# Performance work log

Hardware: AMD Instinct MI355X
Metric: run time of the kernel (lower is better)

The kernel has to match this reference:

```python
import jax, jax.numpy as jnp
import numpy as np
import math

# ---- static config (matches init_kwargs) ----
N_USERS = 40000
N_ITEMS = 30000
N_ENTITIES = 80000
N_REL = 8            # edge_type in [1, N_REL), relation_emb has N_REL-1 rows
DIM = 64
N_HEADS = 2
D_K = DIM // N_HEADS
N_HOPS = 2
E_KG = 800000
E_UI = 600000


def setup_inputs() -> dict:
    key = jax.random.key(0)
    ks = jax.random.split(key, 10)
    return {
        "user_emb": jax.random.normal(ks[0], (N_USERS, DIM), jnp.float32) * 0.1,
        "entity_emb": jax.random.normal(ks[1], (N_ENTITIES, DIM), jnp.float32) * 0.1,
        "relation_emb": jax.random.normal(ks[2], (N_REL - 1, DIM), jnp.float32) * 0.1,
        "W_Q": jax.random.normal(ks[3], (DIM, DIM), jnp.float32) * (1.0 / math.sqrt(DIM)),
        "inter_edge_w": jax.random.uniform(ks[4], (E_UI,), jnp.float32),
        "edge_head": jax.random.randint(ks[5], (E_KG,), 0, N_ENTITIES, jnp.int32),
        "edge_tail": jax.random.randint(ks[6], (E_KG,), 0, N_ENTITIES, jnp.int32),
        "edge_type": jax.random.randint(ks[7], (E_KG,), 1, N_REL, jnp.int32),
        "inter_user": jax.random.randint(ks[8], (E_UI,), 0, N_USERS, jnp.int32),
        "inter_item": jax.random.randint(ks[9], (E_UI,), 0, N_ENTITIES, jnp.int32),
    }


def _seg_softmax(x, seg, n):
    """Numerically-stable softmax over edges grouped by segment id (scatter_softmax)."""
    m = jax.ops.segment_max(x, seg, num_segments=n)
    m = jnp.where(jnp.isneginf(m), 0.0, m)          # empty segments
    ex = jnp.exp(x - m[seg])
    s = jax.ops.segment_sum(ex, seg, num_segments=n)
    return ex / (s[seg] + 1e-16)


def _edge_attn(entity_emb, relation_emb, W_Q, head, tail, etype):
    """Per-edge multi-head attention logits: q_h . (k_h * rel_h) / sqrt(d_k). [E, H]"""
    q = (entity_emb[head] @ W_Q).reshape(-1, N_HEADS, D_K)
    k = (entity_emb[tail] @ W_Q).reshape(-1, N_HEADS, D_K)
    k = k * relation_emb[etype - 1].reshape(-1, N_HEADS, D_K)
    return (q * k).sum(-1) * (1.0 / math.sqrt(D_K))


def _l2norm(x):
    return x / jnp.maximum(jnp.linalg.norm(x, axis=-1, keepdims=True), 1e-12)


def reference(user_emb, entity_emb, relation_emb, W_Q, inter_edge_w,
              edge_head, edge_tail, edge_type, inter_user, inter_item):
    # ---- norm_attn_computer (logits detached in original torch code) ----
    logits = jax.lax.stop_gradient(
        _edge_attn(entity_emb, relation_emb, W_Q, edge_head, edge_tail, edge_type).mean(-1))  # [E]
    score = _seg_softmax(logits, edge_head, N_ENTITIES)
    deg = jax.ops.segment_sum(jnp.ones((E_KG,), jnp.float32), edge_head, num_segments=N_ENTITIES)
    edge_attn_score = score * deg[edge_head]                                   # [E]
    item_attn_sumed = (jax.ops.segment_sum(logits, edge_head, num_segments=N_ENTITIES)
                       + jax.ops.segment_sum(logits, edge_tail, num_segments=N_ENTITIES))[:N_ITEMS]

    # ---- HGT message passing hops (mess_dropout=False) ----
    e, u = entity_emb, user_emb
    e_res, u_res = entity_emb, user_emb
    for _ in range(N_HOPS):
        attn = _edge_attn(e, relation_emb, W_Q, edge_head, edge_tail, edge_type)  # [E, H]
        s = _seg_softmax(attn, edge_head, N_ENTITIES)                              # [E, H]
        neigh = (e[edge_tail] * relation_emb[edge_type - 1]).reshape(-1, N_HEADS, D_K) * s[..., None]
        e_agg = jax.ops.segment_sum(neigh.reshape(-1, DIM), edge_head, num_segments=N_ENTITIES)
        # bipartite user<->item aggregation with interaction weights
        u_agg = jax.ops.segment_sum(inter_edge_w[:, None] * e[inter_item], inter_user,
                                    num_segments=N_USERS)
        e_agg = e_agg + jax.ops.segment_sum(inter_edge_w[:, None] * u[inter_user], inter_item,
                                            num_segments=N_ENTITIES)
        e, u = _l2norm(e_agg), _l2norm(u_agg)
        e_res, u_res = e_res + e, u_res + u

    node_res_emb = jnp.concatenate([u_res, e_res], axis=0)   # [N_USERS+N_ENTITIES, DIM]
    return node_res_emb, edge_attn_score, item_attn_sumed
```

## Files before the change

### kernel.cpp

```cpp
#include <hip/hip_runtime.h>
#include <math.h>

#define NUSERS 40000
#define NENT   80000
#define NITEMS 30000
#define DIM    64
#define EKG    800000
#define EUI    600000
#define NTOT   (NENT + NUSERS + NENT)
#define UBASE  NENT
#define IBASE  (NENT + NUSERS)

struct __align__(8) us4 { unsigned short x, y, z, w; };
static __device__ __forceinline__ float b2f(unsigned short b) {
    return __uint_as_float(((unsigned)b) << 16);
}
static __device__ __forceinline__ unsigned short f2b(float f) {
    unsigned u = __float_as_uint(f);
    return (unsigned short)((u + 0x7FFFu + ((u >> 16) & 1u)) >> 16);
}
static __device__ __forceinline__ float4 ld4b(const unsigned short* p) {
    us4 v = *(const us4*)p;
    return make_float4(b2f(v.x), b2f(v.y), b2f(v.z), b2f(v.w));
}
static __device__ __forceinline__ void st4b(unsigned short* p, float a, float b, float c, float d) {
    us4 v = {f2b(a), f2b(b), f2b(c), f2b(d)};
    *(us4*)p = v;
}

static __device__ __forceinline__ float grp16_sum(float v) {
    v += __shfl_xor(v, 1);
    v += __shfl_xor(v, 2);
    v += __shfl_xor(v, 4);
    v += __shfl_xor(v, 8);
    return v;
}

__global__ void count_kernel(const int* __restrict__ ehead, const int* __restrict__ etail,
                             const int* __restrict__ etype,
                             const int* __restrict__ iuser, const int* __restrict__ iitem,
                             int* __restrict__ cnt,
                             int* __restrict__ hrK, int* __restrict__ hrU, int* __restrict__ hrI,
                             int* __restrict__ tpack) {
    int e = blockIdx.x * blockDim.x + threadIdx.x;
    if (e < EKG) {
        int h = __builtin_nontemporal_load(&ehead[e]);
        int r = atomicAdd(&cnt[h], 1);
        hrK[e] = (h << 15) | r;
        tpack[e] = __builtin_nontemporal_load(&etail[e]) |
                   ((__builtin_nontemporal_load(&etype[e]) - 1) << 20);
    }
    if (e < EUI) {
        int u = __builtin_nontemporal_load(&iuser[e]);
        int r = atomicAdd(&cnt[UBASE + u], 1);
        hrU[e] = (u << 16) | r;
        int it = __builtin_nontemporal_load(&iitem[e]);
        int r2 = atomicAdd(&cnt[IBASE + it], 1);
        hrI[e] = (it << 15) | r2;
    }
}

#define SCHUNK 2048
#define SBLOCKS ((NTOT + SCHUNK - 1) / SCHUNK)

__global__ void scanA_kernel(const int* __restrict__ cnt, int* __restrict__ bsum) {
    int b = blockIdx.x, tid = threadIdx.x;
    int base = b * SCHUNK + tid * 8;
    int ts = 0;
#pragma unroll
    for (int k = 0; k < 8; k++) {
        int i = base + k;
        ts += (i < NTOT) ? cnt[i] : 0;
    }
#pragma unroll
    for (int d = 1; d < 64; d <<= 1) ts += __shfl_xor(ts, d);
    __shared__ int ws[4];
    if ((tid & 63) == 0) ws[tid >> 6] = ts;
    __syncthreads();
    if (tid == 0) bsum[b] = ws[0] + ws[1] + ws[2] + ws[3];
}

__global__ void scanB_kernel(const int* __restrict__ bsum, int* __restrict__ bpre,
                             int* __restrict__ off) {
    int lane = threadIdx.x;
    int carry = 0;
    for (int base = 0; base < SBLOCKS; base += 64) {
        int i = base + lane;
        int x = (i < SBLOCKS) ? bsum[i] : 0;
        int inc = x;
#pragma unroll
        for (int d = 1; d < 64; d <<= 1) {
            int t = __shfl_up(inc, d);
            if (lane >= d) inc += t;
        }
        if (i < SBLOCKS) bpre[i] = carry + inc - x;
        carry += __shfl(inc, 63);
    }
    if (lane == 0) off[NTOT] = carry;
}

__global__ void scanC_kernel(const int* __restrict__ cnt, const int* __restrict__ bpre,
                             int* __restrict__ off) {
    __shared__ int wtot[4];
    int b = blockIdx.x, tid = threadIdx.x, lane = tid & 63, wid = tid >> 6;
    int base = b * SCHUNK + tid * 8;
    int vals[8];
    int ts = 0;
#pragma unroll
    for (int k = 0; k < 8; k++) {
        int i = base + k;
        int x = (i < NTOT) ? cnt[i] : 0;
        vals[k] = ts;
        ts += x;
    }
    int inc = ts;
#pragma unroll
    for (int d = 1; d < 64; d <<= 1) {
        int t = __shfl_up(inc, d);
        if (lane >= d) inc += t;
    }
    if (lane == 63) wtot[wid] = inc;
    __syncthreads();
    int wbase = 0;
    for (int w = 0; w < wid; w++) wbase += wtot[w];
    int tbase = bpre[b] + wbase + (inc - ts);
#pragma unroll
    for (int k = 0; k < 8; k++) {
        int i = base + k;
        if (i < NTOT) off[i] = tbase + vals[k];
    }
}

__global__ void fillKG_kernel(const int* __restrict__ hrK, const int* __restrict__ tpack,
                              const int* __restrict__ off,
                              int* __restrict__ tt, int* __restrict__ eid, int lo, int hi) {
    int e = blockIdx.x * blockDim.x + threadIdx.x;
    if (e >= EKG) return;
    int v = __builtin_nontemporal_load(&hrK[e]);
    int h = ((unsigned)v) >> 15;
    if (h < (unsigned)lo || h >= (unsigned)hi) return;
    int p = off[h] + (v & 0x7FFF);
    tt[p] = __builtin_nontemporal_load(&tpack[e]);
    eid[p] = e;
}

__global__ void fillUIu_kernel(const int* __restrict__ hrU, const int* __restrict__ iitem,
                               const float* __restrict__ iwin, const int* __restrict__ off,
                               int2* __restrict__ upack, int lo, int hi) {
    int e = blockIdx.x * blockDim.x + threadIdx.x;
    if (e >= EUI) return;
    int v = __builtin_nontemporal_load(&hrU[e]);
    int u = ((unsigned)v) >> 16;
    if (u < (unsigned)lo || u >= (unsigned)hi) return;
    int p = off[UBASE + u] - EKG + (v & 0xFFFF);
    upack[p] = make_int2(__builtin_nontemporal_load(&iitem[e]),
                         __float_as_int(__builtin_nontemporal_load(&iwin[e])));
}

__global__ void fillUIi_kernel(const int* __restrict__ hrI, const int* __restrict__ iuser,
                               const float* __restrict__ iwin, const int* __restrict__ off,
                               int2* __restrict__ ipack, int lo, int hi) {
    int e = blockIdx.x * blockDim.x + threadIdx.x;
    if (e >= EUI) return;
    int v = __builtin_nontemporal_load(&hrI[e]);
    int it = ((unsigned)v) >> 15;
    if (it < (unsigned)lo || it >= (unsigned)hi) return;
    int p = off[IBASE + it] - (EKG + EUI) + (v & 0x7FFF);
    ipack[p] = make_int2(__builtin_nontemporal_load(&iuser[e]),
                         __float_as_int(__builtin_nontemporal_load(&iwin[e])));
}

__global__ void cvt_kernel(const float* __restrict__ in, unsigned short* __restrict__ out,
                           int n4) {
    int i = blockIdx.x * blockDim.x + threadIdx.x;
    if (i >= n4) return;
    float4 v = *(const float4*)(in + (size_t)i * 4);
    st4b(out + (size_t)i * 4, v.x, v.y, v.z, v.w);
}

template <int MODE>
__global__ void gemm_wq_kernel(const float* __restrict__ Xf,
                               const unsigned short* __restrict__ Xb_in,
                               const float* __restrict__ W,
                               unsigned short* __restrict__ Pb,
                               unsigned short* __restrict__ Xb_out) {
    __shared__ float Wl[64 * 64];
    int tid = threadIdx.x;
    for (int i = tid; i < 64 * 64; i += 256) Wl[i] = W[i];
    __syncthreads();
    int rloc = tid >> 4;
    int c4 = (tid & 15) * 4;
    int row = blockIdx.x * 16 + rloc;
    float ax = 0, ay = 0, az = 0, aw = 0;
#pragma unroll 8
    for (int d = 0; d < 64; d++) {
        float xv = (MODE == 0) ? Xf[(size_t)row * DIM + d] : b2f(Xb_in[(size_t)row * DIM + d]);
        const float4 w = *(const float4*)&Wl[d * 64 + c4];
        ax += xv * w.x;
        ay += xv * w.y;
        az += xv * w.z;
        aw += xv * w.w;
    }
    st4b(Pb + (size_t)row * DIM + c4, ax, ay, az, aw);
    if (MODE == 0) {
        const float4 xx = *(const float4*)(Xf + (size_t)row * DIM + c4);
        st4b(Xb_out + (size_t)row * DIM + c4, xx.x, xx.y, xx.z, xx.w);
    }
}

template <bool HOP0>
__global__ void hop_kernel(const unsigned short* __restrict__ Pb,
                           const unsigned short* __restrict__ eb,
                           const unsigned short* __restrict__ ub,
                           const float* __restrict__ rel,
                           const int* __restrict__ off,
                           const int* __restrict__ tt, const int* __restrict__ eid,
                           const int2* __restrict__ upack, const int2* __restrict__ ipack,
                           const float* __restrict__ ebase, const float* __restrict__ ubase,
                           const unsigned short* __restrict__ eprevb,
                           const unsigned short* __restrict__ uprevb,
                           float* __restrict__ e_res, float* __restrict__ u_res,
                           unsigned short* __restrict__ enxtb, unsigned short* __restrict__ unxtb,
                           float* __restrict__ logit, float* __restrict__ edge_score,
                           float* __restrict__ item_sum) {
    __shared__ float srel[7 * DIM];
    int tid = threadIdx.x;
    for (int i = tid; i < 7 * DIM; i += 256) srel[i] = rel[i];
    __syncthreads();
    int g = tid >> 4, l = tid & 15;
    int v = blockIdx.x * 16 + g;
    const float sc = 0.17677669529663687f;
    float ax = 0, ay = 0, az = 0, aw = 0;

    if (v < NENT) {
        int o0 = off[v], o1 = off[v + 1];
        int deg = o1 - o0;
        const float4 q = ld4b(Pb + (size_t)v * DIM + l * 4);
        float s_h = 0.f;
        float s_lm = 0.f, lsum = 0.f;
        for (int j = o0; j < o1; j++) {
            unsigned t = (unsigned)tt[j];
            int tail = t & 0xFFFFF;
            int r = t >> 20;
            const float4 k = ld4b(Pb + (size_t)tail * DIM + l * 4);
            const float4 ev = ld4b(eb + (size_t)tail * DIM + l * 4);
            const float4 rv = *(const float4*)(srel + r * DIM + l * 4);
            float part = q.x * k.x * rv.x + q.y * k.y * rv.y + q.z * k.z * rv.z + q.w * k.w * rv.w;
            part += __shfl_xor(part, 1);
            part += __shfl_xor(part, 2);
            part += __shfl_xor(part, 4);
            part *= sc;
            float w = __expf(part);
            s_h += w;
            ax += w * ev.x * rv.x;
            ay += w * ev.y * rv.y;
            az += w * ev.z * rv.z;
            aw += w * ev.w * rv.w;
            if (HOP0) {
                float other = __shfl_xor(part, 8);
                float lm = 0.5f * (part + other);
                s_lm += __expf(lm);
                lsum += lm;
                if (l == 0) {
                    logit[j] = lm;
                    if (tail < NITEMS) atomicAdd(&item_sum[tail], lm);
                }
            }
        }
        float inv_sh = 1.0f / (s_h + 1e-16f);
        ax *= inv_sh;
        ay *= inv_sh;
        az *= inv_sh;
        aw *= inv_sh;
        if (HOP0) {
            if (l == 0 && v < NITEMS && deg > 0) atomicAdd(&item_sum[v], lsum);
            float inv_slm = 1.0f / (s_lm + 1e-16f);
            float degf = (float)deg;
            for (int j = o0 + l; j < o1; j += 16) {
                edge_score[eid[j]] = __expf(logit[j]) * inv_slm * degf;
            }
        }
        int p0 = off[IBASE + v] - (EKG + EUI);
        int p1 = off[IBASE + v + 1] - (EKG + EUI);
        for (int j = p0; j < p1; j++) {
            int2 up = ipack[j];
            float w = __int_as_float(up.y);
            const float4 uv = ld4b(ub + (size_t)up.x * DIM + l * 4);
            ax += w * uv.x;
            ay += w * uv.y;
            az += w * uv.z;
            aw += w * uv.w;
        }
        float nsq = grp16_sum(ax * ax + ay * ay + az * az + aw * aw);
        float invn = 1.0f / fmaxf(sqrtf(nsq), 1e-12f);
        float ox = ax * invn, oy = ay * invn, oz = az * invn, ow = aw * invn;
        size_t base = (size_t)v * DIM + l * 4;
        if (HOP0) {
            st4b(enxtb + base, ox, oy, oz, ow);
        } else {
            const float4 b0 = *(const float4*)(ebase + base);
            const float4 p0v = ld4b(eprevb + base);
            float4 ro = {b0.x + p0v.x + ox, b0.y + p0v.y + oy, b0.z + p0v.z + oz,
                         b0.w + p0v.w + ow};
            *(float4*)(e_res + base) = ro;
        }
    } else {
        int u = v - NENT;
        int p0 = off[UBASE + u] - EKG;
        int p1 = off[UBASE + u + 1] - EKG;
        for (int j = p0; j < p1; j++) {
            int2 up = upack[j];
            float w = __int_as_float(up.y);
            const float4 ev = ld4b(eb + (size_t)up.x * DIM + l * 4);
            ax += w * ev.x;
            ay += w * ev.y;
            az += w * ev.z;
            aw += w * ev.w;
        }
        float nsq = grp16_sum(ax * ax + ay * ay + az * az + aw * aw);
        float invn = 1.0f / fmaxf(sqrtf(nsq), 1e-12f);
        float ox = ax * invn, oy = ay * invn, oz = az * invn, ow = aw * invn;
        size_t base = (size_t)u * DIM + l * 4;
        if (HOP0) {
            st4b(unxtb + base, ox, oy, oz, ow);
        } else {
            const float4 b0 = *(const float4*)(ubase + base);
            const float4 p0v = ld4b(uprevb + base);
            float4 ro = {b0.x + p0v.x + ox, b0.y + p0v.y + oy, b0.z + p0v.z + oz,
                         b0.w + p0v.w + ow};
            *(float4*)(u_res + base) = ro;
        }
    }
}

extern "C" void kernel_launch(void* const* d_in, const int* in_sizes, int n_in,
                              void* d_out, int out_size, void* d_ws, size_t ws_size,
                              hipStream_t stream) {
    const float* user_emb   = (const float*)d_in[0];
    const float* entity_emb = (const float*)d_in[1];
    const float* rel        = (const float*)d_in[2];
    const float* W_Q        = (const float*)d_in[3];
    const float* iwin       = (const float*)d_in[4];
    const int* ehead        = (const int*)d_in[5];
    const int* etail        = (const int*)d_in[6];
    const int* etype        = (const int*)d_in[7];
    const int* iuser        = (const int*)d_in[8];
    const int* iitem        = (const int*)d_in[9];

    float* out        = (float*)d_out;
    float* u_res      = out;
    float* e_res      = out + (size_t)NUSERS * DIM;
    float* edge_score = out + (size_t)(NUSERS + NENT) * DIM;
    float* item_sum   = edge_score + EKG;

    char* w = (char*)d_ws;
    auto alloc = [&](size_t bytes) -> void* {
        void* p = (void*)w;
        w += (bytes + 255) & ~(size_t)255;
        return p;
    };
    unsigned short* Pb  = (unsigned short*)alloc((size_t)NENT * DIM * 2);
    unsigned short* e0b = (unsigned short*)alloc((size_t)NENT * DIM * 2);
    unsigned short* eAb = (unsigned short*)alloc((size_t)NENT * DIM * 2);
    unsigned short* u0b = (unsigned short*)alloc((size_t)NUSERS * DIM * 2);
    unsigned short* uAb = (unsigned short*)alloc((size_t)NUSERS * DIM * 2);
    int* tt      = (int*)alloc((size_t)EKG * 4);
    int* eid     = (int*)alloc((size_t)EKG * 4);
    int2* upack  = (int2*)alloc((size_t)EUI * 8);
    int2* ipack  = (int2*)alloc((size_t)EUI * 8);
    int* hrK     = (int*)alloc((size_t)EKG * 4);
    int* hrU     = (int*)alloc((size_t)EUI * 4);
    int* hrI     = (int*)alloc((size_t)EUI * 4);
    int* tpack   = (int*)alloc((size_t)EKG * 4);
    float* logit = (float*)alloc((size_t)EKG * 4);
    int* cnt     = (int*)alloc((size_t)NTOT * 4);
    int* off     = (int*)alloc((size_t)(NTOT + 1) * 4);
    int* bsum    = (int*)alloc((size_t)SBLOCKS * 4);
    int* bpre    = (int*)alloc((size_t)SBLOCKS * 4);
    (void)ws_size; (void)in_sizes; (void)n_in; (void)out_size;

    hipMemsetAsync(cnt, 0, (size_t)NTOT * 4, stream);
    hipMemsetAsync(item_sum, 0, (size_t)NITEMS * 4, stream);

    count_kernel<<<(EKG + 255) / 256, 256, 0, stream>>>(ehead, etail, etype, iuser, iitem, cnt,
                                                        hrK, hrU, hrI, tpack);
    scanA_kernel<<<SBLOCKS, 256, 0, stream>>>(cnt, bsum);
    scanB_kernel<<<1, 64, 0, stream>>>(bsum, bpre, off);
    scanC_kernel<<<SBLOCKS, 256, 0, stream>>>(cnt, bpre, off);

    const int KGG = (EKG + 255) / 256, UIG = (EUI + 255) / 256;
    for (int p = 0; p < 2; p++)
        fillKG_kernel<<<KGG, 256, 0, stream>>>(hrK, tpack, off, tt, eid,
                                               p * 40000, (p + 1) * 40000);
    for (int p = 0; p < 2; p++)
        fillUIu_kernel<<<UIG, 256, 0, stream>>>(hrU, iitem, iwin, off, upack,
                                                p * 20000, (p + 1) * 20000);
    for (int p = 0; p < 2; p++)
        fillUIi_kernel<<<UIG, 256, 0, stream>>>(hrI, iuser, iwin, off, ipack,
                                                p * 40000, (p + 1) * 40000);

    cvt_kernel<<<(NUSERS * DIM / 4 + 255) / 256, 256, 0, stream>>>(user_emb, u0b,
                                                                   NUSERS * DIM / 4);

    const int HOPG = (NENT + NUSERS) / 16;

    gemm_wq_kernel<0><<<NENT / 16, 256, 0, stream>>>(entity_emb, nullptr, W_Q, Pb, e0b);
    hop_kernel<true><<<HOPG, 256, 0, stream>>>(Pb, e0b, u0b, rel, off, tt, eid, upack, ipack,
                                               nullptr, nullptr, nullptr, nullptr, nullptr,
                                               nullptr, eAb, uAb, logit, edge_score, item_sum);

    gemm_wq_kernel<1><<<NENT / 16, 256, 0, stream>>>(nullptr, eAb, W_Q, Pb, nullptr);
    hop_kernel<false><<<HOPG, 256, 0, stream>>>(Pb, eAb, uAb, rel, off, tt, eid, upack, ipack,
                                                entity_emb, user_emb, eAb, uAb, e_res, u_res,
                                                nullptr, nullptr, nullptr, nullptr, nullptr);
}
```

Measured before the change: 385.8 us.

## Fuse CSR build into one cooperative kernel and split node edges across four slots

Replaces the separate count, scan, fill and convert kernels plus memsets with a single cooperative-launch kernel that uses grid-wide syncs between phases. This removes many kernel launch gaps. The hop kernel now gives each node a full wavefront: four 16-lane slots each take a strided share of the node's edges, and the partial sums are combined with cross-slot shuffles. This raises memory-level parallelism per node, at the cost of lower thread utilisation for low-degree nodes. Grid syncs and a fixed grid of 1024 blocks may serialize the build phases and depend on every block being resident at once.

```diff
diff --git a/kernel.cpp b/kernel.cpp
--- a/kernel.cpp
+++ b/kernel.cpp
@@ -1,5 +1,8 @@
 #include <hip/hip_runtime.h>
+#include <hip/hip_cooperative_groups.h>
 #include <math.h>
+
+namespace cg = cooperative_groups;
 
 #define NUSERS 40000
 #define NENT   80000
@@ -11,6 +14,10 @@
 #define UBASE  NENT
 #define IBASE  (NENT + NUSERS)
 
+#define CGRID    1024
+#define CTHREADS 256
+#define CCHUNK   196
+
 struct __align__(8) us4 { unsigned short x, y, z, w; };
 static __device__ __forceinline__ float b2f(unsigned short b) {
     return __uint_as_float(((unsigned)b) << 16);
@@ -36,146 +43,133 @@
     return v;
 }
 
-__global__ void count_kernel(const int* __restrict__ ehead, const int* __restrict__ etail,
-                             const int* __restrict__ etype,
-                             const int* __restrict__ iuser, const int* __restrict__ iitem,
-                             int* __restrict__ cnt,
-                             int* __restrict__ hrK, int* __restrict__ hrU, int* __restrict__ hrI,
-                             int* __restrict__ tpack) {
-    int e = blockIdx.x * blockDim.x + threadIdx.x;
-    if (e < EKG) {
-        int h = __builtin_nontemporal_load(&ehead[e]);
+__global__ void __launch_bounds__(CTHREADS, 4)
+csr_coop_kernel(const int* __restrict__ ehead, const int* __restrict__ etail,
+                const int* __restrict__ etype, const int* __restrict__ iuser,
+                const int* __restrict__ iitem, const float* __restrict__ iwin,
+                const float* __restrict__ user_emb,
+                int* __restrict__ cnt, int* __restrict__ hrK, int* __restrict__ hrU,
+                int* __restrict__ hrI, int* __restrict__ tpack,
+                int* __restrict__ bsum, int* __restrict__ bpre, int* __restrict__ off,
+                int* __restrict__ tt, int* __restrict__ eid,
+                int2* __restrict__ upack, int2* __restrict__ ipack,
+                unsigned short* __restrict__ u0b, float* __restrict__ item_sum) {
+    cg::grid_group grid = cg::this_grid();
+    __shared__ int ws[4];
+    int tid = threadIdx.x, lane = tid & 63, wid = tid >> 6;
+    int gtid = blockIdx.x * CTHREADS + tid;
+    const int gstride = CGRID * CTHREADS;
+
+    for (int i = gtid; i < NTOT; i += gstride) cnt[i] = 0;
+    for (int i = gtid; i < NITEMS; i += gstride) item_sum[i] = 0.f;
+    grid.sync();
+
+    for (int e = gtid; e < EKG; e += gstride) {
+        int h = ehead[e];
         int r = atomicAdd(&cnt[h], 1);
         hrK[e] = (h << 15) | r;
-        tpack[e] = __builtin_nontemporal_load(&etail[e]) |
-                   ((__builtin_nontemporal_load(&etype[e]) - 1) << 20);
-    }
-    if (e < EUI) {
-        int u = __builtin_nontemporal_load(&iuser[e]);
+        tpack[e] = etail[e] | ((etype[e] - 1) << 20);
+    }
+    for (int e = gtid; e < EUI; e += gstride) {
+        int u = iuser[e];
         int r = atomicAdd(&cnt[UBASE + u], 1);
         hrU[e] = (u << 16) | r;
-        int it = __builtin_nontemporal_load(&iitem[e]);
+        int it = iitem[e];
         int r2 = atomicAdd(&cnt[IBASE + it], 1);
         hrI[e] = (it << 15) | r2;
     }
-}
-
-#define SCHUNK 2048
-#define SBLOCKS ((NTOT + SCHUNK - 1) / SCHUNK)
-
-__global__ void scanA_kernel(const int* __restrict__ cnt, int* __restrict__ bsum) {
-    int b = blockIdx.x, tid = threadIdx.x;
-    int base = b * SCHUNK + tid * 8;
-    int ts = 0;
+    for (int i = gtid; i < NUSERS * (DIM / 4); i += gstride) {
+        float4 vv = *(const float4*)(user_emb + (size_t)i * 4);
+        st4b(u0b + (size_t)i * 4, vv.x, vv.y, vv.z, vv.w);
+    }
+    grid.sync();
+
+    {
+        int base = blockIdx.x * CCHUNK;
+        int s = 0;
+        for (int k = tid; k < CCHUNK; k += CTHREADS) {
+            int i = base + k;
+            s += (i < NTOT) ? cnt[i] : 0;
+        }
 #pragma unroll
-    for (int k = 0; k < 8; k++) {
-        int i = base + k;
-        ts += (i < NTOT) ? cnt[i] : 0;
-    }
+        for (int d = 1; d < 64; d <<= 1) s += __shfl_xor(s, d);
+        if (lane == 0) ws[wid] = s;
+        __syncthreads();
+        if (tid == 0) bsum[blockIdx.x] = ws[0] + ws[1] + ws[2] + ws[3];
+    }
+    grid.sync();
+
+    if (blockIdx.x == 0 && tid < 64) {
+        int carry = 0;
+        for (int base = 0; base < CGRID; base += 64) {
+            int x = bsum[base + lane];
+            int inc = x;
 #pragma unroll
-    for (int d = 1; d < 64; d <<= 1) ts += __shfl_xor(ts, d);
-    __shared__ int ws[4];
-    if ((tid & 63) == 0) ws[tid >> 6] = ts;
-    __syncthreads();
-    if (tid == 0) bsum[b] = ws[0] + ws[1] + ws[2] + ws[3];
-}
-
-__global__ void scanB_kernel(const int* __restrict__ bsum, int* __restrict__ bpre,
-                             int* __restrict__ off) {
-    int lane = threadIdx.x;
-    int carry = 0;
-    for (int base = 0; base < SBLOCKS; base += 64) {
-        int i = base + lane;
-        int x = (i < SBLOCKS) ? bsum[i] : 0;
+            for (int d = 1; d < 64; d <<= 1) {
+                int t = __shfl_up(inc, d);
+                if (lane >= d) inc += t;
+            }
+            bpre[base + lane] = carry + inc - x;
+            carry += __shfl(inc, 63);
+        }
+        if (lane == 0) off[NTOT] = carry;
+    }
+    grid.sync();
+
+    {
+        __syncthreads();
+        int base = blockIdx.x * CCHUNK;
+        int i = base + tid;
+        int x = (tid < CCHUNK && i < NTOT) ? cnt[i] : 0;
         int inc = x;
 #pragma unroll
         for (int d = 1; d < 64; d <<= 1) {
             int t = __shfl_up(inc, d);
             if (lane >= d) inc += t;
         }
-        if (i < SBLOCKS) bpre[i] = carry + inc - x;
-        carry += __shfl(inc, 63);
-    }
-    if (lane == 0) off[NTOT] = carry;
-}
-
-__global__ void scanC_kernel(const int* __restrict__ cnt, const int* __restrict__ bpre,
-                             int* __restrict__ off) {
-    __shared__ int wtot[4];
-    int b = blockIdx.x, tid = threadIdx.x, lane = tid & 63, wid = tid >> 6;
-    int base = b * SCHUNK + tid * 8;
-    int vals[8];
-    int ts = 0;
-#pragma unroll
-    for (int k = 0; k < 8; k++) {
-        int i = base + k;
-        int x = (i < NTOT) ? cnt[i] : 0;
-        vals[k] = ts;
-        ts += x;
-    }
-    int inc = ts;
-#pragma unroll
-    for (int d = 1; d < 64; d <<= 1) {
-        int t = __shfl_up(inc, d);
-        if (lane >= d) inc += t;
-    }
-    if (lane == 63) wtot[wid] = inc;
-    __syncthreads();
-    int wbase = 0;
-    for (int w = 0; w < wid; w++) wbase += wtot[w];
-    int tbase = bpre[b] + wbase + (inc - ts);
-#pragma unroll
-    for (int k = 0; k < 8; k++) {
-        int i = base + k;
-        if (i < NTOT) off[i] = tbase + vals[k];
-    }
-}
-
-__global__ void fillKG_kernel(const int* __restrict__ hrK, const int* __restrict__ tpack,
-                              const int* __restrict__ off,
-                              int* __restrict__ tt, int* __restrict__ eid, int lo, int hi) {
-    int e = blockIdx.x * blockDim.x + threadIdx.x;
-    if (e >= EKG) return;
-    int v = __builtin_nontemporal_load(&hrK[e]);
-    int h = ((unsigned)v) >> 15;
-    if (h < (unsigned)lo || h >= (unsigned)hi) return;
-    int p = off[h] + (v & 0x7FFF);
-    tt[p] = __builtin_nontemporal_load(&tpack[e]);
-    eid[p] = e;
-}
-
-__global__ void fillUIu_kernel(const int* __restrict__ hrU, const int* __restrict__ iitem,
-                               const float* __restrict__ iwin, const int* __restrict__ off,
-                               int2* __restrict__ upack, int lo, int hi) {
-    int e = blockIdx.x * blockDim.x + threadIdx.x;
-    if (e >= EUI) return;
-    int v = __builtin_nontemporal_load(&hrU[e]);
-    int u = ((unsigned)v) >> 16;
-    if (u < (unsigned)lo || u >= (unsigned)hi) return;
-    int p = off[UBASE + u] - EKG + (v & 0xFFFF);
-    upack[p] = make_int2(__builtin_nontemporal_load(&iitem[e]),
-                         __float_as_int(__builtin_nontemporal_load(&iwin[e])));
-}
-
-__global__ void fillUIi_kernel(const int* __restrict__ hrI, const int* __restrict__ iuser,
-                               const float* __restrict__ iwin, const int* __restrict__ off,
-                               int2* __restrict__ ipack, int lo, int hi) {
-    int e = blockIdx.x * blockDim.x + threadIdx.x;
-    if (e >= EUI) return;
-    int v = __builtin_nontemporal_load(&hrI[e]);
-    int it = ((unsigned)v) >> 15;
-    if (it < (unsigned)lo || it >= (unsigned)hi) return;
-    int p = off[IBASE + it] - (EKG + EUI) + (v & 0x7FFF);
-    ipack[p] = make_int2(__builtin_nontemporal_load(&iuser[e]),
-                         __float_as_int(__builtin_nontemporal_load(&iwin[e])));
-}
-
-__global__ void cvt_kernel(const float* __restrict__ in, unsigned short* __restrict__ out,
-                           int n4) {
-    int i = blockIdx.x * blockDim.x + threadIdx.x;
-    if (i >= n4) return;
-    float4 v = *(const float4*)(in + (size_t)i * 4);
-    st4b(out + (size_t)i * 4, v.x, v.y, v.z, v.w);
+        if (lane == 63) ws[wid] = inc;
+        __syncthreads();
+        int wb = 0;
+        for (int w = 0; w < wid; w++) wb += ws[w];
+        int excl = bpre[blockIdx.x] + wb + (inc - x);
+        if (tid < CCHUNK && i < NTOT) off[i] = excl;
+    }
+    grid.sync();
+
+    for (int p = 0; p < 2; p++) {
+        unsigned lo = p * 40000u, hi = lo + 40000u;
+        for (int e = gtid; e < EKG; e += gstride) {
+            unsigned vpk = (unsigned)hrK[e];
+            unsigned h = vpk >> 15;
+            if (h < lo || h >= hi) continue;
+            int pp = off[h] + (vpk & 0x7FFF);
+            tt[pp] = tpack[e];
+            eid[pp] = e;
+        }
+        grid.sync();
+    }
+    for (int p = 0; p < 2; p++) {
+        unsigned lo = p * 20000u, hi = lo + 20000u;
+        for (int e = gtid; e < EUI; e += gstride) {
+            unsigned vpk = (unsigned)hrU[e];
+            unsigned u = vpk >> 16;
+            if (u < lo || u >= hi) continue;
+            int pp = off[UBASE + u] - EKG + (vpk & 0xFFFF);
+            upack[pp] = make_int2(iitem[e], __float_as_int(iwin[e]));
+        }
+        grid.sync();
+    }
+    for (int p = 0; p < 2; p++) {
+        unsigned lo = p * 40000u, hi = lo + 40000u;
+        for (int e = gtid; e < EUI; e += gstride) {
+            unsigned vpk = (unsigned)hrI[e];
+            unsigned it = vpk >> 15;
+            if (it < lo || it >= hi) continue;
+            int pp = off[IBASE + it] - (EKG + EUI) + (vpk & 0x7FFF);
+            ipack[pp] = make_int2(iuser[e], __float_as_int(iwin[e]));
+        }
+        if (p == 0) grid.sync();
+    }
 }
 
 template <int MODE>
@@ -208,6 +202,7 @@
     }
 }
 
+#define XRED(x) { x += __shfl_xor(x, 16); x += __shfl_xor(x, 32); }
 template <bool HOP0>
 __global__ void hop_kernel(const unsigned short* __restrict__ Pb,
                            const unsigned short* __restrict__ eb,
@@ -227,18 +222,19 @@
     int tid = threadIdx.x;
     for (int i = tid; i < 7 * DIM; i += 256) srel[i] = rel[i];
     __syncthreads();
-    int g = tid >> 4, l = tid & 15;
-    int v = blockIdx.x * 16 + g;
+    int lane = tid & 63;
+    int slot = lane >> 4, l = lane & 15;
+    int v = blockIdx.x * 4 + (tid >> 6);
     const float sc = 0.17677669529663687f;
     float ax = 0, ay = 0, az = 0, aw = 0;
+    float bx = 0, by = 0, bz = 0, bw = 0;
 
     if (v < NENT) {
         int o0 = off[v], o1 = off[v + 1];
         int deg = o1 - o0;
         const float4 q = ld4b(Pb + (size_t)v * DIM + l * 4);
-        float s_h = 0.f;
-        float s_lm = 0.f, lsum = 0.f;
-        for (int j = o0; j < o1; j++) {
+        float s_h = 0.f, s_lm = 0.f, lsum = 0.f;
+        for (int j = o0 + slot; j < o1; j += 4) {
             unsigned t = (unsigned)tt[j];
             int tail = t & 0xFFFFF;
             int r = t >> 20;
@@ -267,68 +263,76 @@
                 }
             }
         }
-        float inv_sh = 1.0f / (s_h + 1e-16f);
-        ax *= inv_sh;
-        ay *= inv_sh;
-        az *= inv_sh;
-        aw *= inv_sh;
-        if (HOP0) {
-            if (l == 0 && v < NITEMS && deg > 0) atomicAdd(&item_sum[v], lsum);
-            float inv_slm = 1.0f / (s_lm + 1e-16f);
-            float degf = (float)deg;
-            for (int j = o0 + l; j < o1; j += 16) {
-                edge_score[eid[j]] = __expf(logit[j]) * inv_slm * degf;
-            }
-        }
         int p0 = off[IBASE + v] - (EKG + EUI);
         int p1 = off[IBASE + v + 1] - (EKG + EUI);
-        for (int j = p0; j < p1; j++) {
+        for (int j = p0 + slot; j < p1; j += 4) {
             int2 up = ipack[j];
             float w = __int_as_float(up.y);
             const float4 uv = ld4b(ub + (size_t)up.x * DIM + l * 4);
-            ax += w * uv.x;
-            ay += w * uv.y;
-            az += w * uv.z;
-            aw += w * uv.w;
-        }
-        float nsq = grp16_sum(ax * ax + ay * ay + az * az + aw * aw);
+            bx += w * uv.x;
+            by += w * uv.y;
+            bz += w * uv.z;
+            bw += w * uv.w;
+        }
+        XRED(ax) XRED(ay) XRED(az) XRED(aw)
+        XRED(bx) XRED(by) XRED(bz) XRED(bw)
+        XRED(s_h)
+        float inv_sh = 1.0f / (s_h + 1e-16f);
+        float ox = ax * inv_sh + bx;
+        float oy = ay * inv_sh + by;
+        float oz = az * inv_sh + bz;
+        float ow = aw * inv_sh + bw;
+        if (HOP0) {
+            XRED(s_lm) XRED(lsum)
+            if (lane == 0 && deg > 0 && v < NITEMS) atomicAdd(&item_sum[v], lsum);
+            float inv_slm = 1.0f / (s_lm + 1e-16f);
+            float degf = (float)deg;
+            for (int j = o0 + lane; j < o1; j += 64)
+                edge_score[eid[j]] = __expf(logit[j]) * inv_slm * degf;
+        }
+        float nsq = grp16_sum(ox * ox + oy * oy + oz * oz + ow * ow);
         float invn = 1.0f / fmaxf(sqrtf(nsq), 1e-12f);
-        float ox = ax * invn, oy = ay * invn, oz = az * invn, ow = aw * invn;
-        size_t base = (size_t)v * DIM + l * 4;
-        if (HOP0) {
-            st4b(enxtb + base, ox, oy, oz, ow);
-        } else {
-            const float4 b0 = *(const float4*)(ebase + base);
-            const float4 p0v = ld4b(eprevb + base);
-            float4 ro = {b0.x + p0v.x + ox, b0.y + p0v.y + oy, b0.z + p0v.z + oz,
-                         b0.w + p0v.w + ow};
-            *(float4*)(e_res + base) = ro;
+        ox *= invn; oy *= invn; oz *= invn; ow *= invn;
+        if (slot == 0) {
+            size_t base = (size_t)v * DIM + l * 4;
+            if (HOP0) {
+                st4b(enxtb + base, ox, oy, oz, ow);
+            } else {
+                const float4 b0 = *(const float4*)(ebase + base);
+                const float4 pv = ld4b(eprevb + base);
+                float4 ro = {b0.x + pv.x + ox, b0.y + pv.y + oy, b0.z + pv.z + oz,
+                             b0.w + pv.w + ow};
+                *(float4*)(e_res + base) = ro;
+            }
         }
     } else {
         int u = v - NENT;
         int p0 = off[UBASE + u] - EKG;
         int p1 = off[UBASE + u + 1] - EKG;
-        for (int j = p0; j < p1; j++) {
+        for (int j = p0 + slot; j < p1; j += 4) {
             int2 up = upack[j];
             float w = __int_as_float(up.y);
             const float4 ev = ld4b(eb + (size_t)up.x * DIM + l * 4);
-            ax += w * ev.x;
-            ay += w * ev.y;
-            az += w * ev.z;
-            aw += w * ev.w;
-        }
-        float nsq = grp16_sum(ax * ax + ay * ay + az * az + aw * aw);
+            bx += w * ev.x;
+            by += w * ev.y;
+            bz += w * ev.z;
+            bw += w * ev.w;
+        }
+        XRED(bx) XRED(by) XRED(bz) XRED(bw)
+        float nsq = grp16_sum(bx * bx + by * by + bz * bz + bw * bw);
         float invn = 1.0f / fmaxf(sqrtf(nsq), 1e-12f);
-        float ox = ax * invn, oy = ay * invn, oz = az * invn, ow = aw * invn;
-        size_t base = (size_t)u * DIM + l * 4;
-        if (HOP0) {
-            st4b(unxtb + base, ox, oy, oz, ow);
-        } else {
-            const float4 b0 = *(const float4*)(ubase + base);
-            const float4 p0v = ld4b(uprevb + base);
-            float4 ro = {b0.x + p0v.x + ox, b0.y + p0v.y + oy, b0.z + p0v.z + oz,
-                         b0.w + p0v.w + ow};
-            *(float4*)(u_res + base) = ro;
+        float ox = bx * invn, oy = by * invn, oz = bz * invn, ow = bw * invn;
+        if (slot == 0) {
+            size_t base = (size_t)u * DIM + l * 4;
+            if (HOP0) {
+                st4b(unxtb + base, ox, oy, oz, ow);
+            } else {
+                const float4 b0 = *(const float4*)(ubase + base);
+                const float4 pv = ld4b(uprevb + base);
+                float4 ro = {b0.x + pv.x + ox, b0.y + pv.y + oy, b0.z + pv.z + oz,
+                             b0.w + pv.w + ow};
+                *(float4*)(u_res + base) = ro;
+            }
         }
     }
 }
@@ -375,34 +379,20 @@
     float* logit = (float*)alloc((size_t)EKG * 4);
     int* cnt     = (int*)alloc((size_t)NTOT * 4);
     int* off     = (int*)alloc((size_t)(NTOT + 1) * 4);
-    int* bsum    = (int*)alloc((size_t)SBLOCKS * 4);
-    int* bpre    = (int*)alloc((size_t)SBLOCKS * 4);
+    int* bsum    = (int*)alloc((size_t)CGRID * 4);
+    int* bpre    = (int*)alloc((size_t)CGRID * 4);
     (void)ws_size; (void)in_sizes; (void)n_in; (void)out_size;
 
-    hipMemsetAsync(cnt, 0, (size_t)NTOT * 4, stream);
-    hipMemsetAsync(item_sum, 0, (size_t)NITEMS * 4, stream);
-
-    count_kernel<<<(EKG + 255) / 256, 256, 0, stream>>>(ehead, etail, etype, iuser, iitem, cnt,
-                                                        hrK, hrU, hrI, tpack);
-    scanA_kernel<<<SBLOCKS, 256, 0, stream>>>(cnt, bsum);
-    scanB_kernel<<<1, 64, 0, stream>>>(bsum, bpre, off);
-    scanC_kernel<<<SBLOCKS, 256, 0, stream>>>(cnt, bpre, off);
-
-    const int KGG = (EKG + 255) / 256, UIG = (EUI + 255) / 256;
-    for (int p = 0; p < 2; p++)
-        fillKG_kernel<<<KGG, 256, 0, stream>>>(hrK, tpack, off, tt, eid,
-                                               p * 40000, (p + 1) * 40000);
-    for (int p = 0; p < 2; p++)
-        fillUIu_kernel<<<UIG, 256, 0, stream>>>(hrU, iitem, iwin, off, upack,
-                                                p * 20000, (p + 1) * 20000);
-    for (int p = 0; p < 2; p++)
-        fillUIi_kernel<<<UIG, 256, 0, stream>>>(hrI, iuser, iwin, off, ipack,
-                                                p * 40000, (p + 1) * 40000);
-
-    cvt_kernel<<<(NUSERS * DIM / 4 + 255) / 256, 256, 0, stream>>>(user_emb, u0b,
-                                                                   NUSERS * DIM / 4);
-
-    const int HOPG = (NENT + NUSERS) / 16;
+    void* cargs[] = {(void*)&ehead, (void*)&etail, (void*)&etype, (void*)&iuser, (void*)&iitem,
+                     (void*)&iwin,  (void*)&user_emb,
+                     (void*)&cnt,   (void*)&hrK,   (void*)&hrU,   (void*)&hrI,   (void*)&tpack,
+                     (void*)&bsum,  (void*)&bpre,  (void*)&off,
+                     (void*)&tt,    (void*)&eid,   (void*)&upack, (void*)&ipack,
+                     (void*)&u0b,   (void*)&item_sum};
+    hipLaunchCooperativeKernel((void*)csr_coop_kernel, dim3(CGRID), dim3(CTHREADS), cargs, 0,
+                               stream);
+
+    const int HOPG = (NENT + NUSERS) / 4;
 
     gemm_wq_kernel<0><<<NENT / 16, 256, 0, stream>>>(entity_emb, nullptr, W_Q, Pb, e0b);
     hop_kernel<true><<<HOPG, 256, 0, stream>>>(Pb, e0b, u0b, rel, off, tt, eid, upack, ipack,
```

Result: slower. 1.482 ms (+284.1%).

## Split each node's edge list across four 16-lane slots; fold user cvt into count kernel

Applied to the files above, without the earlier changes.

The hop kernel now gives each node a full 64-lane wavefront instead of a 16-lane group. The four 16-lane slots stride over the node's KG and UI edges, and partial sums (aggregates, softmax denominators, logit sums) are combined with cross-slot shuffles before normalization. Only slot 0 writes the result. This is meant to raise memory-level parallelism and shorten the serial per-edge loop on gather-bound hops, at the cost of four times more blocks and extra shuffle reductions. Separately, the user-embedding bf16 conversion is merged into the count kernel to drop one launch.

```diff
diff --git a/kernel.cpp b/kernel.cpp
--- a/kernel.cpp
+++ b/kernel.cpp
@@ -39,9 +39,10 @@
 __global__ void count_kernel(const int* __restrict__ ehead, const int* __restrict__ etail,
                              const int* __restrict__ etype,
                              const int* __restrict__ iuser, const int* __restrict__ iitem,
+                             const float* __restrict__ user_emb,
                              int* __restrict__ cnt,
                              int* __restrict__ hrK, int* __restrict__ hrU, int* __restrict__ hrI,
-                             int* __restrict__ tpack) {
+                             int* __restrict__ tpack, unsigned short* __restrict__ u0b) {
     int e = blockIdx.x * blockDim.x + threadIdx.x;
     if (e < EKG) {
         int h = __builtin_nontemporal_load(&ehead[e]);
@@ -57,6 +58,10 @@
         int it = __builtin_nontemporal_load(&iitem[e]);
         int r2 = atomicAdd(&cnt[IBASE + it], 1);
         hrI[e] = (it << 15) | r2;
+    }
+    if (e < NUSERS * (DIM / 4)) {
+        float4 vv = *(const float4*)(user_emb + (size_t)e * 4);
+        st4b(u0b + (size_t)e * 4, vv.x, vv.y, vv.z, vv.w);
     }
 }
 
@@ -168,14 +173,6 @@
     int p = off[IBASE + it] - (EKG + EUI) + (v & 0x7FFF);
     ipack[p] = make_int2(__builtin_nontemporal_load(&iuser[e]),
                          __float_as_int(__builtin_nontemporal_load(&iwin[e])));
-}
-
-__global__ void cvt_kernel(const float* __restrict__ in, unsigned short* __restrict__ out,
-                           int n4) {
-    int i = blockIdx.x * blockDim.x + threadIdx.x;
-    if (i >= n4) return;
-    float4 v = *(const float4*)(in + (size_t)i * 4);
-    st4b(out + (size_t)i * 4, v.x, v.y, v.z, v.w);
 }
 
 template <int MODE>
@@ -208,6 +205,7 @@
     }
 }
 
+#define XRED(x) { x += __shfl_xor(x, 16); x += __shfl_xor(x, 32); }
 template <bool HOP0>
 __global__ void hop_kernel(const unsigned short* __restrict__ Pb,
                            const unsigned short* __restrict__ eb,
@@ -227,18 +225,19 @@
     int tid = threadIdx.x;
     for (int i = tid; i < 7 * DIM; i += 256) srel[i] = rel[i];
     __syncthreads();
-    int g = tid >> 4, l = tid & 15;
-    int v = blockIdx.x * 16 + g;
+    int lane = tid & 63;
+    int slot = lane >> 4, l = lane & 15;
+    int v = blockIdx.x * 4 + (tid >> 6);
     const float sc = 0.17677669529663687f;
     float ax = 0, ay = 0, az = 0, aw = 0;
+    float bx = 0, by = 0, bz = 0, bw = 0;
 
     if (v < NENT) {
         int o0 = off[v], o1 = off[v + 1];
         int deg = o1 - o0;
         const float4 q = ld4b(Pb + (size_t)v * DIM + l * 4);
-        float s_h = 0.f;
-        float s_lm = 0.f, lsum = 0.f;
-        for (int j = o0; j < o1; j++) {
+        float s_h = 0.f, s_lm = 0.f, lsum = 0.f;
+        for (int j = o0 + slot; j < o1; j += 4) {
             unsigned t = (unsigned)tt[j];
             int tail = t & 0xFFFFF;
             int r = t >> 20;
@@ -267,68 +266,76 @@
                 }
             }
         }
-        float inv_sh = 1.0f / (s_h + 1e-16f);
-        ax *= inv_sh;
-        ay *= inv_sh;
-        az *= inv_sh;
-        aw *= inv_sh;
-        if (HOP0) {
-            if (l == 0 && v < NITEMS && deg > 0) atomicAdd(&item_sum[v], lsum);
-            float inv_slm = 1.0f / (s_lm + 1e-16f);
-            float degf = (float)deg;
-            for (int j = o0 + l; j < o1; j += 16) {
-                edge_score[eid[j]] = __expf(logit[j]) * inv_slm * degf;
-            }
-        }
         int p0 = off[IBASE + v] - (EKG + EUI);
         int p1 = off[IBASE + v + 1] - (EKG + EUI);
-        for (int j = p0; j < p1; j++) {
+        for (int j = p0 + slot; j < p1; j += 4) {
             int2 up = ipack[j];
             float w = __int_as_float(up.y);
             const float4 uv = ld4b(ub + (size_t)up.x * DIM + l * 4);
-            ax += w * uv.x;
-            ay += w * uv.y;
-            az += w * uv.z;
-            aw += w * uv.w;
-        }
-        float nsq = grp16_sum(ax * ax + ay * ay + az * az + aw * aw);
+            bx += w * uv.x;
+            by += w * uv.y;
+            bz += w * uv.z;
+            bw += w * uv.w;
+        }
+        XRED(ax) XRED(ay) XRED(az) XRED(aw)
+        XRED(bx) XRED(by) XRED(bz) XRED(bw)
+        XRED(s_h)
+        float inv_sh = 1.0f / (s_h + 1e-16f);
+        float ox = ax * inv_sh + bx;
+        float oy = ay * inv_sh + by;
+        float oz = az * inv_sh + bz;
+        float ow = aw * inv_sh + bw;
+        if (HOP0) {
+            XRED(s_lm) XRED(lsum)
+            if (lane == 0 && deg > 0 && v < NITEMS) atomicAdd(&item_sum[v], lsum);
+            float inv_slm = 1.0f / (s_lm + 1e-16f);
+            float degf = (float)deg;
+            for (int j = o0 + lane; j < o1; j += 64)
+                edge_score[eid[j]] = __expf(logit[j]) * inv_slm * degf;
+        }
+        float nsq = grp16_sum(ox * ox + oy * oy + oz * oz + ow * ow);
         float invn = 1.0f / fmaxf(sqrtf(nsq), 1e-12f);
-        float ox = ax * invn, oy = ay * invn, oz = az * invn, ow = aw * invn;
-        size_t base = (size_t)v * DIM + l * 4;
-        if (HOP0) {
-            st4b(enxtb + base, ox, oy, oz, ow);
-        } else {
-            const float4 b0 = *(const float4*)(ebase + base);
-            const float4 p0v = ld4b(eprevb + base);
-            float4 ro = {b0.x + p0v.x + ox, b0.y + p0v.y + oy, b0.z + p0v.z + oz,
-                         b0.w + p0v.w + ow};
-            *(float4*)(e_res + base) = ro;
+        ox *= invn; oy *= invn; oz *= invn; ow *= invn;
+        if (slot == 0) {
+            size_t base = (size_t)v * DIM + l * 4;
+            if (HOP0) {
+                st4b(enxtb + base, ox, oy, oz, ow);
+            } else {
+                const float4 b0 = *(const float4*)(ebase + base);
+                const float4 pv = ld4b(eprevb + base);
+                float4 ro = {b0.x + pv.x + ox, b0.y + pv.y + oy, b0.z + pv.z + oz,
+                             b0.w + pv.w + ow};
+                *(float4*)(e_res + base) = ro;
+            }
         }
     } else {
         int u = v - NENT;
         int p0 = off[UBASE + u] - EKG;
         int p1 = off[UBASE + u + 1] - EKG;
-        for (int j = p0; j < p1; j++) {
+        for (int j = p0 + slot; j < p1; j += 4) {
             int2 up = upack[j];
             float w = __int_as_float(up.y);
             const float4 ev = ld4b(eb + (size_t)up.x * DIM + l * 4);
-            ax += w * ev.x;
-            ay += w * ev.y;
-            az += w * ev.z;
-            aw += w * ev.w;
-        }
-        float nsq = grp16_sum(ax * ax + ay * ay + az * az + aw * aw);
+            bx += w * ev.x;
+            by += w * ev.y;
+            bz += w * ev.z;
+            bw += w * ev.w;
+        }
+        XRED(bx) XRED(by) XRED(bz) XRED(bw)
+        float nsq = grp16_sum(bx * bx + by * by + bz * bz + bw * bw);
         float invn = 1.0f / fmaxf(sqrtf(nsq), 1e-12f);
-        float ox = ax * invn, oy = ay * invn, oz = az * invn, ow = aw * invn;
-        size_t base = (size_t)u * DIM + l * 4;
-        if (HOP0) {
-            st4b(unxtb + base, ox, oy, oz, ow);
-        } else {
-            const float4 b0 = *(const float4*)(ubase + base);
-            const float4 p0v = ld4b(uprevb + base);
-            float4 ro = {b0.x + p0v.x + ox, b0.y + p0v.y + oy, b0.z + p0v.z + oz,
-                         b0.w + p0v.w + ow};
-            *(float4*)(u_res + base) = ro;
+        float ox = bx * invn, oy = by * invn, oz = bz * invn, ow = bw * invn;
+        if (slot == 0) {
+            size_t base = (size_t)u * DIM + l * 4;
+            if (HOP0) {
+                st4b(unxtb + base, ox, oy, oz, ow);
+            } else {
+                const float4 b0 = *(const float4*)(ubase + base);
+                const float4 pv = ld4b(uprevb + base);
+                float4 ro = {b0.x + pv.x + ox, b0.y + pv.y + oy, b0.z + pv.z + oz,
+                             b0.w + pv.w + ow};
+                *(float4*)(u_res + base) = ro;
+            }
         }
     }
 }
@@ -382,8 +389,8 @@
     hipMemsetAsync(cnt, 0, (size_t)NTOT * 4, stream);
     hipMemsetAsync(item_sum, 0, (size_t)NITEMS * 4, stream);
 
-    count_kernel<<<(EKG + 255) / 256, 256, 0, stream>>>(ehead, etail, etype, iuser, iitem, cnt,
-                                                        hrK, hrU, hrI, tpack);
+    count_kernel<<<(EKG + 255) / 256, 256, 0, stream>>>(ehead, etail, etype, iuser, iitem,
+                                                        user_emb, cnt, hrK, hrU, hrI, tpack, u0b);
     scanA_kernel<<<SBLOCKS, 256, 0, stream>>>(cnt, bsum);
     scanB_kernel<<<1, 64, 0, stream>>>(bsum, bpre, off);
     scanC_kernel<<<SBLOCKS, 256, 0, stream>>>(cnt, bpre, off);
@@ -399,10 +406,7 @@
         fillUIi_kernel<<<UIG, 256, 0, stream>>>(hrI, iuser, iwin, off, ipack,
                                                 p * 40000, (p + 1) * 40000);
 
-    cvt_kernel<<<(NUSERS * DIM / 4 + 255) / 256, 256, 0, stream>>>(user_emb, u0b,
-                                                                   NUSERS * DIM / 4);
-
-    const int HOPG = (NENT + NUSERS) / 16;
+    const int HOPG = (NENT + NUSERS) / 4;
 
     gemm_wq_kernel<0><<<NENT / 16, 256, 0, stream>>>(entity_emb, nullptr, W_Q, Pb, e0b);
     hop_kernel<true><<<HOPG, 256, 0, stream>>>(Pb, e0b, u0b, rel, off, tt, eid, upack, ipack,
```

After: 419.2 us. +8.7%, slower.
